# Performance work log

Hardware: AMD Instinct MI355X
Metric: run time of the kernel (lower is better)

The kernel has to match this reference:

```python
import jax, jax.numpy as jnp
import numpy as np

B, C, H, W = 8, 256, 64, 64
S = 2            # area_size = sqrt(num_areas)
A = S * S        # num_areas
NH = 8           # num_heads (hardcoded in module)
EPS = 1e-5       # nn.LayerNorm default eps


def setup_inputs() -> dict:
    key = jax.random.key(0)
    ks = jax.random.split(key, 4)
    scale = 0.02
    return {
        "x": jax.random.normal(ks[0], (B, C, H, W), jnp.float32),
        "W_in": jax.random.normal(ks[1], (A, 3 * C, C), jnp.float32) * scale,
        "b_in": jnp.zeros((A, 3 * C), jnp.float32),
        "W_out": jax.random.normal(ks[2], (A, C, C), jnp.float32) * scale,
        "b_out": jnp.zeros((A, C), jnp.float32),
        "gamma": jnp.ones((C,), jnp.float32),
        "beta": jnp.zeros((C,), jnp.float32),
    }


def reference(x, W_in, b_in, W_out, b_out, gamma, beta):
    b, c, h, w = x.shape
    ah, aw = h // S, w // S
    L = ah * aw
    dh = c // NH

    # split into 2x2 areas, flatten each to a sequence: [B, A, L, C]
    # area index = i*S + j (row-major), matching the torch loop order
    xa = (x.reshape(b, c, S, ah, S, aw)
            .transpose(0, 2, 4, 3, 5, 1)   # [B, i, j, ah, aw, C]
            .reshape(b, A, L, c))

    # per-area in-projection (torch Linear: y = x @ W^T + b)
    qkv = jnp.einsum('balc,adc->bald', xa, W_in) + b_in[None, :, None, :]
    q, k, v = jnp.split(qkv, 3, axis=-1)
    q = q.reshape(b, A, L, NH, dh)
    k = k.reshape(b, A, L, NH, dh)
    v = v.reshape(b, A, L, NH, dh)

    scale = jnp.asarray(dh, x.dtype) ** -0.5
    scores = jnp.einsum('balhd,bamhd->bahlm', q * scale, k)  # [B,A,NH,L,L]
    attn = jax.nn.softmax(scores, axis=-1)
    o = jnp.einsum('bahlm,bamhd->balhd', attn, v).reshape(b, A, L, c)
    o = jnp.einsum('balc,adc->bald', o, W_out) + b_out[None, :, None, :]

    # residual + shared LayerNorm over channel dim
    y = o + xa
    mu = jnp.mean(y, axis=-1, keepdims=True)
    var = jnp.mean((y - mu) ** 2, axis=-1, keepdims=True)
    y = (y - mu) * jax.lax.rsqrt(var + EPS) * gamma + beta

    # reassemble areas back to [B, C, H, W]
    out = (y.reshape(b, S, S, ah, aw, c)
             .transpose(0, 5, 1, 3, 2, 4)  # [B, C, i, ah, j, aw]
             .reshape(b, c, h, w))
    return out
```

## Files before the change

kernel.cpp:

```cpp
#include <hip/hip_runtime.h>
#include <cstdint>
#include <cstddef>

#define B_    8
#define C_    256
#define H_    64
#define W_    64
#define A_    4
#define NH_   8
#define DH_   32
#define L_    1024
#define NPAIR 32
#define QKVN  768

typedef __bf16 bf16;
typedef __bf16 bf16x8 __attribute__((ext_vector_type(8)));
typedef __bf16 bf16x4 __attribute__((ext_vector_type(4)));
typedef float  f32x4  __attribute__((ext_vector_type(4)));

#define QSCALE 0.25506866729736328f

__device__ inline f32x4 mfma16(bf16x8 a, bf16x8 b, f32x4 c) {
    return __builtin_amdgcn_mfma_f32_16x16x32_bf16(a, b, c, 0, 0, 0);
}
__device__ inline bf16x8 ld8(const bf16* p) { return *(const bf16x8*)p; }

__device__ inline void stage16(const bf16* g, bf16* l) {
    __builtin_amdgcn_global_load_lds(
        (const __attribute__((address_space(1))) void*)g,
        (__attribute__((address_space(3))) void*)l, 16, 0, 0);
}

#define NW4 (786432 / 4)
#define NO4 (262144 / 4)
__global__ __launch_bounds__(256) void k_split(const float* __restrict__ x,
                                               bf16* __restrict__ xa,
                                               const float* __restrict__ Win,
                                               const float* __restrict__ Wout,
                                               bf16* __restrict__ Winb,
                                               bf16* __restrict__ Woutb) {
    __shared__ float lds[32][257];
    int bid = blockIdx.x;
    int t = threadIdx.x;
    if (bid >= NPAIR * 32) {
        int tid = (bid - NPAIR * 32) * 256 + t;
        if (tid < NW4) {
            float4 v = ((const float4*)Win)[tid];
            bf16x4 ov = {(bf16)v.x, (bf16)v.y, (bf16)v.z, (bf16)v.w};
            ((bf16x4*)Winb)[tid] = ov;
        } else if (tid < NW4 + NO4) {
            int t2 = tid - NW4;
            float4 v = ((const float4*)Wout)[t2];
            bf16x4 ov = {(bf16)v.x, (bf16)v.y, (bf16)v.z, (bf16)v.w};
            ((bf16x4*)Woutb)[t2] = ov;
        }
        return;
    }
    int pair = bid >> 5, p = bid & 31;
    int b = pair >> 2, a = pair & 3, i = a >> 1, j = a & 1;
    int q = t & 31, csub = t >> 5;
    const float* xb = x + (size_t)b * C_ * H_ * W_ + (size_t)(i * 32 + p) * W_ + j * 32;
    for (int r = 0; r < 32; ++r) {
        int c = r * 8 + csub;
        lds[q][c] = xb[(size_t)c * H_ * W_ + q];
    }
    __syncthreads();
    bf16* xr = xa + ((size_t)pair * L_ + (size_t)p * 32) * C_;
    for (int r = 0; r < 32; ++r) {
        xr[(size_t)r * C_ + t] = (bf16)lds[r][t];
    }
}

__global__ __launch_bounds__(256) void k_qkv(const bf16* __restrict__ xa,
                                             const bf16* __restrict__ Win,
                                             const float* __restrict__ bin,
                                             bf16* __restrict__ qk,
                                             bf16* __restrict__ vT) {
    __shared__ __align__(16) char smem[32768];
    bf16* lA = (bf16*)smem;
    bf16* lB = (bf16*)(smem + 16384);
    int bid = blockIdx.x;
    int nt = bid % 6, mt = (bid / 6) & 7, pair = bid / 48;
    int a = pair & 3;
    int t = threadIdx.x, w = t >> 6, lane = t & 63;
    int wm = w >> 1, wn = w & 1;
    int quad = lane >> 4, l16 = lane & 15;
    int m0 = mt * 128, n0 = nt * 128;
    int r8 = lane >> 3, pc = lane & 7, jj = pc ^ r8;
    const bf16* ga = xa + (size_t)pair * L_ * C_ + (size_t)(m0 + w * 32 + r8) * C_ + jj * 8;
    const bf16* gb = Win + (size_t)a * QKVN * C_ + (size_t)(n0 + w * 32 + r8) * C_ + jj * 8;
    f32x4 acc[4][4];
#pragma unroll
    for (int fm = 0; fm < 4; ++fm)
#pragma unroll
        for (int fn = 0; fn < 4; ++fn) acc[fm][fn] = (f32x4){0.f, 0.f, 0.f, 0.f};
#pragma unroll
    for (int i = 0; i < 4; ++i) {
        stage16(ga + (size_t)(i * 8) * C_, lA + (w * 32 + i * 8) * 64);
        stage16(gb + (size_t)(i * 8) * C_, lB + (w * 32 + i * 8) * 64);
    }
    for (int k0 = 0; k0 < C_; k0 += 64) {
        __syncthreads();
        bf16x8 am[2][4], bn[2][4];
#pragma unroll
        for (int ks = 0; ks < 2; ++ks) {
            int p = (ks * 4 + quad) ^ (l16 & 7);
#pragma unroll
            for (int f = 0; f < 4; ++f) {
                am[ks][f] = *(const bf16x8*)&lA[(wm * 64 + f * 16 + l16) * 64 + p * 8];
                bn[ks][f] = *(const bf16x8*)&lB[(wn * 64 + f * 16 + l16) * 64 + p * 8];
            }
        }
        __syncthreads();
        if (k0 + 64 < C_) {
            int kn = k0 + 64;
#pragma unroll
            for (int i = 0; i < 4; ++i) {
                stage16(ga + (size_t)(i * 8) * C_ + kn, lA + (w * 32 + i * 8) * 64);
                stage16(gb + (size_t)(i * 8) * C_ + kn, lB + (w * 32 + i * 8) * 64);
            }
        }
#pragma unroll
        for (int ks = 0; ks < 2; ++ks)
#pragma unroll
            for (int fm = 0; fm < 4; ++fm)
#pragma unroll
                for (int fn = 0; fn < 4; ++fn)
                    acc[fm][fn] = mfma16(am[ks][fm], bn[ks][fn], acc[fm][fn]);
    }
    int colbase = n0 + wn * 64;
    int mb = m0 + wm * 64;
    __syncthreads();
    bf16* slab = (bf16*)smem + w * 2304;
    float bias[4];
#pragma unroll
    for (int fn = 0; fn < 4; ++fn) bias[fn] = bin[a * QKVN + colbase + fn * 16 + l16];
    int sr = lane >> 3, seg = lane & 7;
    if (colbase < 512) {
        float sc = (colbase < 256) ? QSCALE : 1.0f;
        bf16* ob = qk + (size_t)pair * L_ * 512;
#pragma unroll
        for (int pass = 0; pass < 2; ++pass) {
#pragma unroll
            for (int k = 0; k < 2; ++k) {
                int fm = pass * 2 + k;
#pragma unroll
                for (int fn = 0; fn < 4; ++fn)
#pragma unroll
                    for (int r = 0; r < 4; ++r)
                        slab[(k * 16 + quad * 4 + r) * 72 + fn * 16 + l16] =
                            (bf16)((acc[fm][fn][r] + bias[fn]) * sc);
            }
#pragma unroll
            for (int rr = 0; rr < 4; ++rr) {
                int row = rr * 8 + sr;
                bf16x8 v = *(const bf16x8*)&slab[row * 72 + seg * 8];
                *(bf16x8*)&ob[(size_t)(mb + pass * 32 + row) * 512 + colbase + seg * 8] = v;
            }
        }
    } else {
        bf16* vb = vT + (size_t)pair * C_ * L_;
        int e00 = colbase - 512;
#pragma unroll
        for (int pass = 0; pass < 2; ++pass) {
#pragma unroll
            for (int k = 0; k < 2; ++k) {
                int fn = pass * 2 + k;
#pragma unroll
                for (int fm = 0; fm < 4; ++fm) {
                    bf16x4 pk = {(bf16)(acc[fm][fn][0] + bias[fn]), (bf16)(acc[fm][fn][1] + bias[fn]),
                                 (bf16)(acc[fm][fn][2] + bias[fn]), (bf16)(acc[fm][fn][3] + bias[fn])};
                    *(bf16x4*)&slab[(k * 16 + l16) * 72 + fm * 16 + quad * 4] = pk;
                }
            }
#pragma unroll
            for (int rr = 0; rr < 4; ++rr) {
                int el = rr * 8 + sr;
                bf16x8 v = *(const bf16x8*)&slab[el * 72 + seg * 8];
                *(bf16x8*)&vb[(size_t)(e00 + pass * 32 + el) * L_ + mb + seg * 8] = v;
            }
        }
    }
}

__global__ __launch_bounds__(256) void k_attn(const bf16* __restrict__ qk,
                                              const bf16* __restrict__ vT,
                                              bf16* __restrict__ o) {
    __shared__ __align__(16) bf16 pl[4][1024];
    __shared__ __align__(16) bf16 klds[4 * 512];
    __shared__ __align__(16) bf16 vlds[4 * 512];
    int bid = blockIdx.x;
    int pair = bid & 31, rest = bid >> 5;
    int head = rest & 7, qb = rest >> 3;
    int t = threadIdx.x, w = t >> 6, lane = t & 63, quad = lane >> 4, l16 = lane & 15;
    const bf16* qbp = qk + (size_t)pair * L_ * 512;
    const bf16* kg = qbp + (size_t)(l16 * 4 + w) * 512 + 256 + head * DH_ + quad * 8;
    const bf16* vg = vT + ((size_t)pair * C_ + head * DH_ + (w & 1) * 16 + l16) * L_
                        + (w >> 1) * 32 + quad * 8;
    bf16* kdst = &klds[w * 512];
    bf16* vdst = &vlds[w * 512];
    int qbase = qb * 128 + w * 32;
    bf16x8 qf[2];
    f32x4 acc0[2], acc1[2], l4[2];
#pragma unroll
    for (int f = 0; f < 2; ++f) {
        qf[f] = ld8(qbp + (size_t)(qbase + f * 16 + l16) * 512 + head * DH_ + quad * 8);
        acc0[f] = (f32x4){0.f, 0.f, 0.f, 0.f};
        acc1[f] = (f32x4){0.f, 0.f, 0.f, 0.f};
        l4[f]   = (f32x4){0.f, 0.f, 0.f, 0.f};
    }
    stage16(kg, kdst);
    stage16(vg, vdst);
    __syncthreads();

    for (int kv0 = 0; kv0 < L_; kv0 += 64) {
        bf16x8 kf[4], vf[4];
#pragma unroll
        for (int i = 0; i < 4; ++i) {
            kf[i] = ld8(&klds[(i * 64 + lane) * 8]);
            vf[i] = ld8(&vlds[(i * 64 + lane) * 8]);
        }
        __syncthreads();
        int kvn = (kv0 + 64) & (L_ - 1);
        stage16(kg + (size_t)kvn * 512, kdst);
        stage16(vg + kvn, vdst);
#pragma unroll
        for (int f = 0; f < 2; ++f) {
            f32x4 s[4];
#pragma unroll
            for (int kb = 0; kb < 4; ++kb) s[kb] = mfma16(qf[f], kf[kb], (f32x4){0.f, 0.f, 0.f, 0.f});
            char* pw = (char*)&pl[w][0];
#pragma unroll
            for (int r = 0; r < 4; ++r) {
                float p0 = __builtin_amdgcn_exp2f(s[0][r]);
                float p1 = __builtin_amdgcn_exp2f(s[1][r]);
                float p2 = __builtin_amdgcn_exp2f(s[2][r]);
                float p3 = __builtin_amdgcn_exp2f(s[3][r]);
                l4[f][r] += (p0 + p1) + (p2 + p3);
                bf16x4 pv = {(bf16)p0, (bf16)p1, (bf16)p2, (bf16)p3};
                int row = quad * 4 + r;
                int wo = (row * 128 + l16 * 8) ^ ((row & 7) << 4);
                *(bf16x4*)(pw + wo) = pv;
            }
#pragma unroll
            for (int ks = 0; ks < 2; ++ks) {
                int ro = (l16 * 128 + ks * 64 + quad * 16) ^ ((l16 & 7) << 4);
                bf16x8 pf = *(const bf16x8*)(pw + ro);
                acc0[f] = mfma16(pf, vf[ks * 2 + 0], acc0[f]);
                acc1[f] = mfma16(pf, vf[ks * 2 + 1], acc1[f]);
            }
        }
        __syncthreads();
    }
    bf16* orow = o + (size_t)pair * L_ * C_ + head * DH_;
#pragma unroll
    for (int f = 0; f < 2; ++f) {
#pragma unroll
        for (int r = 0; r < 4; ++r) {
            float s1 = l4[f][r];
#pragma unroll
            for (int off = 1; off < 16; off <<= 1) s1 += __shfl_xor(s1, off);
            float inv = 1.f / s1;
            int row = qbase + f * 16 + quad * 4 + r;
            orow[(size_t)row * C_ + l16]      = (bf16)(acc0[f][r] * inv);
            orow[(size_t)row * C_ + 16 + l16] = (bf16)(acc1[f][r] * inv);
        }
    }
}

__global__ __launch_bounds__(256) void k_out(const bf16* __restrict__ o,
                                             const bf16* __restrict__ Wout,
                                             const float* __restrict__ bout,
                                             const bf16* __restrict__ xa,
                                             const float* __restrict__ gamma,
                                             const float* __restrict__ beta,
                                             float* __restrict__ out) {
    __shared__ __align__(16) char smem[40960];
    bf16* lA = (bf16*)smem;
    bf16* lB = (bf16*)(smem + 8192);
    float* tr = (float*)smem;
    __shared__ float red[2][2][32][2];
    int bid = blockIdx.x;
    int mt = bid & 15, pair = bid >> 4;
    int a = pair & 3;
    int t = threadIdx.x, w = t >> 6, lane = t & 63;
    int wm = w >> 1, wn = w & 1;
    int quad = lane >> 4, l16 = lane & 15;
    int m0 = mt * 64;
    int r8 = lane >> 3, pc = lane & 7, jj = pc ^ r8;
    const bf16* ga = o + (size_t)pair * L_ * C_ + (size_t)(m0 + w * 16 + r8) * C_ + jj * 8;
    const bf16* gb = Wout + (size_t)a * C_ * C_ + (size_t)(w * 64 + r8) * C_ + jj * 8;
    f32x4 acc[2][8];
#pragma unroll
    for (int fm = 0; fm < 2; ++fm)
#pragma unroll
        for (int fn = 0; fn < 8; ++fn) acc[fm][fn] = (f32x4){0.f, 0.f, 0.f, 0.f};
    for (int k0 = 0; k0 < C_; k0 += 64) {
        __syncthreads();
#pragma unroll
        for (int i = 0; i < 2; ++i)
            stage16(ga + (size_t)(i * 8) * C_ + k0, lA + (w * 16 + i * 8) * 64);
#pragma unroll
        for (int i = 0; i < 8; ++i)
            stage16(gb + (size_t)(i * 8) * C_ + k0, lB + (w * 64 + i * 8) * 64);
        __syncthreads();
#pragma unroll
        for (int ks = 0; ks < 2; ++ks) {
            int p = (ks * 4 + quad) ^ (l16 & 7);
            bf16x8 am[2], bn[8];
#pragma unroll
            for (int f = 0; f < 2; ++f)
                am[f] = *(const bf16x8*)&lA[(wm * 32 + f * 16 + l16) * 64 + p * 8];
#pragma unroll
            for (int f = 0; f < 8; ++f)
                bn[f] = *(const bf16x8*)&lB[(wn * 128 + f * 16 + l16) * 64 + p * 8];
#pragma unroll
            for (int fm = 0; fm < 2; ++fm)
#pragma unroll
                for (int fn = 0; fn < 8; ++fn)
                    acc[fm][fn] = mfma16(am[fm], bn[fn], acc[fm][fn]);
        }
    }
    const bf16* xb = xa + ((size_t)pair * L_ + m0 + wm * 32) * C_;
    float g8[8], be8[8];
#pragma unroll
    for (int fn = 0; fn < 8; ++fn) {
        int col = wn * 128 + fn * 16 + l16;
        float bias = bout[a * C_ + col];
        g8[fn] = gamma[col];
        be8[fn] = beta[col];
#pragma unroll
        for (int fm = 0; fm < 2; ++fm)
#pragma unroll
            for (int r = 0; r < 4; ++r)
                acc[fm][fn][r] += bias + (float)xb[(size_t)(fm * 16 + quad * 4 + r) * C_ + col];
    }
#pragma unroll
    for (int fm = 0; fm < 2; ++fm) {
#pragma unroll
        for (int r = 0; r < 4; ++r) {
            float s1 = 0.f, s2 = 0.f;
#pragma unroll
            for (int fn = 0; fn < 8; ++fn) {
                float v = acc[fm][fn][r];
                s1 += v; s2 += v * v;
            }
#pragma unroll
            for (int off = 1; off < 16; off <<= 1) {
                s1 += __shfl_xor(s1, off);
                s2 += __shfl_xor(s2, off);
            }
            if (l16 == 0) {
                int rl = fm * 16 + quad * 4 + r;
                red[wm][wn][rl][0] = s1;
                red[wm][wn][rl][1] = s2;
            }
        }
    }
    __syncthreads();
#pragma unroll
    for (int fm = 0; fm < 2; ++fm) {
#pragma unroll
        for (int r = 0; r < 4; ++r) {
            int rl = fm * 16 + quad * 4 + r;
            float t1 = red[wm][0][rl][0] + red[wm][1][rl][0];
            float t2 = red[wm][0][rl][1] + red[wm][1][rl][1];
            float mu = t1 * (1.f / 256.f);
            float var = t2 * (1.f / 256.f) - mu * mu;
            float rstd = rsqrtf(var + 1e-5f);
#pragma unroll
            for (int fn = 0; fn < 8; ++fn)
                acc[fm][fn][r] = (acc[fm][fn][r] - mu) * rstd * g8[fn] + be8[fn];
        }
    }
    int b = pair >> 2, i = (a >> 1), j = a & 1;
    int q = t & 31, csub = t >> 5;
    float* ob = out + (size_t)b * C_ * H_ * W_ + (size_t)(i * 32 + (m0 >> 5)) * W_ + j * 32;
#pragma unroll
    for (int ch = 0; ch < 2; ++ch) {
        __syncthreads();
        if (wm == ch) {
#pragma unroll
            for (int fm = 0; fm < 2; ++fm) {
                int rb = fm * 16 + quad * 4;
#pragma unroll
                for (int r = 0; r < 4; ++r)
#pragma unroll
                    for (int fn = 0; fn < 8; ++fn)
                        tr[(rb + r) * 258 + wn * 128 + fn * 16 + l16] = acc[fm][fn][r];
            }
        }
        __syncthreads();
#pragma unroll
        for (int r32 = 0; r32 < 32; ++r32) {
            int c = r32 * 8 + csub;
            ob[(size_t)c * (H_ * W_) + (size_t)ch * W_ + q] = tr[q * 258 + c];
        }
    }
}

extern "C" void kernel_launch(void* const* d_in, const int* in_sizes, int n_in,
                              void* d_out, int out_size, void* d_ws, size_t ws_size,
                              hipStream_t stream) {
    (void)in_sizes; (void)n_in; (void)out_size; (void)ws_size;
    const float* x     = (const float*)d_in[0];
    const float* Win   = (const float*)d_in[1];
    const float* bin   = (const float*)d_in[2];
    const float* Wout  = (const float*)d_in[3];
    const float* bout  = (const float*)d_in[4];
    const float* gamma = (const float*)d_in[5];
    const float* beta  = (const float*)d_in[6];
    float* out = (float*)d_out;

    char* ws = (char*)d_ws;
    bf16* xa    = (bf16*)ws;
    bf16* qk    = (bf16*)(ws + ((size_t)16 << 20));
    bf16* vT    = (bf16*)(ws + ((size_t)48 << 20));
    bf16* o     = (bf16*)(ws + ((size_t)64 << 20));
    bf16* Winb  = (bf16*)(ws + ((size_t)80 << 20));
    bf16* Woutb = (bf16*)(ws + ((size_t)82 << 20));

    k_split<<<NPAIR * 32 + 1024, 256, 0, stream>>>(x, xa, Win, Wout, Winb, Woutb);
    k_qkv<<<NPAIR * 8 * 6, 256, 0, stream>>>(xa, Winb, bin, qk, vT);
    k_attn<<<NPAIR * NH_ * 8, 256, 0, stream>>>(qk, vT, o);
    k_out<<<NPAIR * 16, 256, 0, stream>>>(o, Woutb, bout, xa, gamma, beta, out);
}
```

Before: 193.9 us.

## Halve out-projection tile and load GEMM operands directly from global memory

The output projection + LayerNorm kernel now handles 32 rows per block instead of 64, which doubles the grid to 1024 blocks. Its MFMA operands are loaded straight from global memory (ld8) instead of being staged through swizzled shared memory. This removes the per-k-step barriers and LDS staging, and the transpose store now runs in a single pass. In exchange, each block rereads the full Wout slice from global/L2 with less reuse, and the smaller tile halves the MFMA work per operand load.

```diff
diff --git a/kernel.cpp b/kernel.cpp
--- a/kernel.cpp
+++ b/kernel.cpp
@@ -275,53 +275,36 @@
                                              const float* __restrict__ gamma,
                                              const float* __restrict__ beta,
                                              float* __restrict__ out) {
-    __shared__ __align__(16) char smem[40960];
-    bf16* lA = (bf16*)smem;
-    bf16* lB = (bf16*)(smem + 8192);
-    float* tr = (float*)smem;
-    __shared__ float red[2][2][32][2];
+    __shared__ float tr[32 * 258];
+    __shared__ float red[2][2][16][2];
     int bid = blockIdx.x;
-    int mt = bid & 15, pair = bid >> 4;
+    int mt = bid & 31, pair = bid >> 5;
     int a = pair & 3;
     int t = threadIdx.x, w = t >> 6, lane = t & 63;
     int wm = w >> 1, wn = w & 1;
     int quad = lane >> 4, l16 = lane & 15;
-    int m0 = mt * 64;
-    int r8 = lane >> 3, pc = lane & 7, jj = pc ^ r8;
-    const bf16* ga = o + (size_t)pair * L_ * C_ + (size_t)(m0 + w * 16 + r8) * C_ + jj * 8;
-    const bf16* gb = Wout + (size_t)a * C_ * C_ + (size_t)(w * 64 + r8) * C_ + jj * 8;
-    f32x4 acc[2][8];
-#pragma unroll
-    for (int fm = 0; fm < 2; ++fm)
-#pragma unroll
-        for (int fn = 0; fn < 8; ++fn) acc[fm][fn] = (f32x4){0.f, 0.f, 0.f, 0.f};
+    int m0 = mt * 32;
+    const bf16* ga = o + (size_t)pair * L_ * C_ + (size_t)(m0 + wm * 16 + l16) * C_;
+    const bf16* gb = Wout + (size_t)a * C_ * C_ + (size_t)(wn * 128 + l16) * C_;
+    f32x4 acc[8];
+#pragma unroll
+    for (int fn = 0; fn < 8; ++fn) acc[fn] = (f32x4){0.f, 0.f, 0.f, 0.f};
+#pragma unroll 1
     for (int k0 = 0; k0 < C_; k0 += 64) {
-        __syncthreads();
-#pragma unroll
-        for (int i = 0; i < 2; ++i)
-            stage16(ga + (size_t)(i * 8) * C_ + k0, lA + (w * 16 + i * 8) * 64);
-#pragma unroll
-        for (int i = 0; i < 8; ++i)
-            stage16(gb + (size_t)(i * 8) * C_ + k0, lB + (w * 64 + i * 8) * 64);
-        __syncthreads();
 #pragma unroll
         for (int ks = 0; ks < 2; ++ks) {
-            int p = (ks * 4 + quad) ^ (l16 & 7);
-            bf16x8 am[2], bn[8];
-#pragma unroll
-            for (int f = 0; f < 2; ++f)
-                am[f] = *(const bf16x8*)&lA[(wm * 32 + f * 16 + l16) * 64 + p * 8];
+            int kk = k0 + ks * 32 + quad * 8;
+            bf16x8 am = ld8(ga + kk);
+            bf16x8 bn[8];
 #pragma unroll
             for (int f = 0; f < 8; ++f)
-                bn[f] = *(const bf16x8*)&lB[(wn * 128 + f * 16 + l16) * 64 + p * 8];
-#pragma unroll
-            for (int fm = 0; fm < 2; ++fm)
-#pragma unroll
-                for (int fn = 0; fn < 8; ++fn)
-                    acc[fm][fn] = mfma16(am[fm], bn[fn], acc[fm][fn]);
-        }
-    }
-    const bf16* xb = xa + ((size_t)pair * L_ + m0 + wm * 32) * C_;
+                bn[f] = ld8(gb + (size_t)(f * 16) * C_ + kk);
+#pragma unroll
+            for (int fn = 0; fn < 8; ++fn)
+                acc[fn] = mfma16(am, bn[fn], acc[fn]);
+        }
+    }
+    const bf16* xb = xa + ((size_t)pair * L_ + m0 + wm * 16) * C_;
     float g8[8], be8[8];
 #pragma unroll
     for (int fn = 0; fn < 8; ++fn) {
@@ -330,72 +313,50 @@
         g8[fn] = gamma[col];
         be8[fn] = beta[col];
 #pragma unroll
-        for (int fm = 0; fm < 2; ++fm)
-#pragma unroll
-            for (int r = 0; r < 4; ++r)
-                acc[fm][fn][r] += bias + (float)xb[(size_t)(fm * 16 + quad * 4 + r) * C_ + col];
-    }
-#pragma unroll
-    for (int fm = 0; fm < 2; ++fm) {
-#pragma unroll
-        for (int r = 0; r < 4; ++r) {
-            float s1 = 0.f, s2 = 0.f;
-#pragma unroll
-            for (int fn = 0; fn < 8; ++fn) {
-                float v = acc[fm][fn][r];
-                s1 += v; s2 += v * v;
-            }
-#pragma unroll
-            for (int off = 1; off < 16; off <<= 1) {
-                s1 += __shfl_xor(s1, off);
-                s2 += __shfl_xor(s2, off);
-            }
-            if (l16 == 0) {
-                int rl = fm * 16 + quad * 4 + r;
-                red[wm][wn][rl][0] = s1;
-                red[wm][wn][rl][1] = s2;
-            }
-        }
-    }
-    __syncthreads();
-#pragma unroll
-    for (int fm = 0; fm < 2; ++fm) {
-#pragma unroll
-        for (int r = 0; r < 4; ++r) {
-            int rl = fm * 16 + quad * 4 + r;
-            float t1 = red[wm][0][rl][0] + red[wm][1][rl][0];
-            float t2 = red[wm][0][rl][1] + red[wm][1][rl][1];
-            float mu = t1 * (1.f / 256.f);
-            float var = t2 * (1.f / 256.f) - mu * mu;
-            float rstd = rsqrtf(var + 1e-5f);
-#pragma unroll
-            for (int fn = 0; fn < 8; ++fn)
-                acc[fm][fn][r] = (acc[fm][fn][r] - mu) * rstd * g8[fn] + be8[fn];
-        }
-    }
+        for (int r = 0; r < 4; ++r)
+            acc[fn][r] += bias + (float)xb[(size_t)(quad * 4 + r) * C_ + col];
+    }
+#pragma unroll
+    for (int r = 0; r < 4; ++r) {
+        float s1 = 0.f, s2 = 0.f;
+#pragma unroll
+        for (int fn = 0; fn < 8; ++fn) {
+            float v = acc[fn][r];
+            s1 += v; s2 += v * v;
+        }
+#pragma unroll
+        for (int off = 1; off < 16; off <<= 1) {
+            s1 += __shfl_xor(s1, off);
+            s2 += __shfl_xor(s2, off);
+        }
+        if (l16 == 0) {
+            red[wm][wn][quad * 4 + r][0] = s1;
+            red[wm][wn][quad * 4 + r][1] = s2;
+        }
+    }
+    __syncthreads();
+#pragma unroll
+    for (int r = 0; r < 4; ++r) {
+        int rl = quad * 4 + r;
+        float t1 = red[wm][0][rl][0] + red[wm][1][rl][0];
+        float t2 = red[wm][0][rl][1] + red[wm][1][rl][1];
+        float mu = t1 * (1.f / 256.f);
+        float var = t2 * (1.f / 256.f) - mu * mu;
+        float rstd = rsqrtf(var + 1e-5f);
+#pragma unroll
+        for (int fn = 0; fn < 8; ++fn) {
+            float v = (acc[fn][r] - mu) * rstd * g8[fn] + be8[fn];
+            tr[(wm * 16 + rl) * 258 + wn * 128 + fn * 16 + l16] = v;
+        }
+    }
+    __syncthreads();
     int b = pair >> 2, i = (a >> 1), j = a & 1;
     int q = t & 31, csub = t >> 5;
-    float* ob = out + (size_t)b * C_ * H_ * W_ + (size_t)(i * 32 + (m0 >> 5)) * W_ + j * 32;
-#pragma unroll
-    for (int ch = 0; ch < 2; ++ch) {
-        __syncthreads();
-        if (wm == ch) {
-#pragma unroll
-            for (int fm = 0; fm < 2; ++fm) {
-                int rb = fm * 16 + quad * 4;
-#pragma unroll
-                for (int r = 0; r < 4; ++r)
-#pragma unroll
-                    for (int fn = 0; fn < 8; ++fn)
-                        tr[(rb + r) * 258 + wn * 128 + fn * 16 + l16] = acc[fm][fn][r];
-            }
-        }
-        __syncthreads();
-#pragma unroll
-        for (int r32 = 0; r32 < 32; ++r32) {
-            int c = r32 * 8 + csub;
-            ob[(size_t)c * (H_ * W_) + (size_t)ch * W_ + q] = tr[q * 258 + c];
-        }
+    float* ob = out + (size_t)b * C_ * H_ * W_ + (size_t)(i * 32 + mt) * W_ + j * 32;
+#pragma unroll
+    for (int r32 = 0; r32 < 32; ++r32) {
+        int c = r32 * 8 + csub;
+        ob[(size_t)c * (H_ * W_) + q] = tr[q * 258 + c];
     }
 }
 
@@ -423,5 +384,5 @@
     k_split<<<NPAIR * 32 + 1024, 256, 0, stream>>>(x, xa, Win, Wout, Winb, Woutb);
     k_qkv<<<NPAIR * 8 * 6, 256, 0, stream>>>(xa, Winb, bin, qk, vT);
     k_attn<<<NPAIR * NH_ * 8, 256, 0, stream>>>(qk, vT, o);
-    k_out<<<NPAIR * 16, 256, 0, stream>>>(o, Woutb, bout, xa, gamma, beta, out);
-}
+    k_out<<<NPAIR * 32, 256, 0, stream>>>(o, Woutb, bout, xa, gamma, beta, out);
+}
```

Measured after the change: 214.9 us. +10.9%, slower.

## Rewrite attention kernel with 32x32 MFMA and register-resident P via permlane swaps

Applied to the files above, without the earlier changes.

The attention kernel switches from 16x16x32 MFMA tiles with LDS-staged K/V and an LDS round trip for the probability matrix to 32x32x16 MFMA computing S^T. The probabilities are packed to bf16 in registers and rearranged with v_permlane32_swap, so they feed the PV MFMA directly. K and V are now loaded straight from global memory each 32-key step instead of being staged through LDS, and all __syncthreads calls are removed. This is meant to cut LDS traffic and barrier stalls. In exchange, global loads are no longer shared across waves, so the kernel relies on cache hits and has less latency hiding.

```diff
diff --git a/kernel.cpp b/kernel.cpp
--- a/kernel.cpp
+++ b/kernel.cpp
@@ -17,13 +17,27 @@
 typedef __bf16 bf16x8 __attribute__((ext_vector_type(8)));
 typedef __bf16 bf16x4 __attribute__((ext_vector_type(4)));
 typedef float  f32x4  __attribute__((ext_vector_type(4)));
+typedef float  f32x16 __attribute__((ext_vector_type(16)));
+typedef int    i32x4  __attribute__((ext_vector_type(4)));
 
 #define QSCALE 0.25506866729736328f
 
 __device__ inline f32x4 mfma16(bf16x8 a, bf16x8 b, f32x4 c) {
     return __builtin_amdgcn_mfma_f32_16x16x32_bf16(a, b, c, 0, 0, 0);
 }
+__device__ inline f32x16 mfma32(bf16x8 a, bf16x8 b, f32x16 c) {
+    return __builtin_amdgcn_mfma_f32_32x32x16_bf16(a, b, c, 0, 0, 0);
+}
 __device__ inline bf16x8 ld8(const bf16* p) { return *(const bf16x8*)p; }
+
+__device__ inline int cvtpk(float lo, float hi) {
+    int r;
+    asm("v_cvt_pk_bf16_f32 %0, %1, %2" : "=v"(r) : "v"(lo), "v"(hi));
+    return r;
+}
+__device__ inline void swap32(int& a, int& b) {
+    asm volatile("v_permlane32_swap_b32 %0, %1" : "+v"(a), "+v"(b));
+}
 
 __device__ inline void stage16(const bf16* g, bf16* l) {
     __builtin_amdgcn_global_load_lds(
@@ -186,85 +200,62 @@
 __global__ __launch_bounds__(256) void k_attn(const bf16* __restrict__ qk,
                                               const bf16* __restrict__ vT,
                                               bf16* __restrict__ o) {
-    __shared__ __align__(16) bf16 pl[4][1024];
-    __shared__ __align__(16) bf16 klds[4 * 512];
-    __shared__ __align__(16) bf16 vlds[4 * 512];
     int bid = blockIdx.x;
     int pair = bid & 31, rest = bid >> 5;
     int head = rest & 7, qb = rest >> 3;
-    int t = threadIdx.x, w = t >> 6, lane = t & 63, quad = lane >> 4, l16 = lane & 15;
+    int t = threadIdx.x, w = t >> 6, lane = t & 63;
+    int l31 = lane & 31, hi = lane >> 5;
+    int qrow = qb * 128 + w * 32 + l31;
     const bf16* qbp = qk + (size_t)pair * L_ * 512;
-    const bf16* kg = qbp + (size_t)(l16 * 4 + w) * 512 + 256 + head * DH_ + quad * 8;
-    const bf16* vg = vT + ((size_t)pair * C_ + head * DH_ + (w & 1) * 16 + l16) * L_
-                        + (w >> 1) * 32 + quad * 8;
-    bf16* kdst = &klds[w * 512];
-    bf16* vdst = &vlds[w * 512];
-    int qbase = qb * 128 + w * 32;
-    bf16x8 qf[2];
-    f32x4 acc0[2], acc1[2], l4[2];
-#pragma unroll
-    for (int f = 0; f < 2; ++f) {
-        qf[f] = ld8(qbp + (size_t)(qbase + f * 16 + l16) * 512 + head * DH_ + quad * 8);
-        acc0[f] = (f32x4){0.f, 0.f, 0.f, 0.f};
-        acc1[f] = (f32x4){0.f, 0.f, 0.f, 0.f};
-        l4[f]   = (f32x4){0.f, 0.f, 0.f, 0.f};
-    }
-    stage16(kg, kdst);
-    stage16(vg, vdst);
-    __syncthreads();
-
-    for (int kv0 = 0; kv0 < L_; kv0 += 64) {
-        bf16x8 kf[4], vf[4];
-#pragma unroll
-        for (int i = 0; i < 4; ++i) {
-            kf[i] = ld8(&klds[(i * 64 + lane) * 8]);
-            vf[i] = ld8(&vlds[(i * 64 + lane) * 8]);
-        }
-        __syncthreads();
-        int kvn = (kv0 + 64) & (L_ - 1);
-        stage16(kg + (size_t)kvn * 512, kdst);
-        stage16(vg + kvn, vdst);
-#pragma unroll
-        for (int f = 0; f < 2; ++f) {
-            f32x4 s[4];
-#pragma unroll
-            for (int kb = 0; kb < 4; ++kb) s[kb] = mfma16(qf[f], kf[kb], (f32x4){0.f, 0.f, 0.f, 0.f});
-            char* pw = (char*)&pl[w][0];
-#pragma unroll
-            for (int r = 0; r < 4; ++r) {
-                float p0 = __builtin_amdgcn_exp2f(s[0][r]);
-                float p1 = __builtin_amdgcn_exp2f(s[1][r]);
-                float p2 = __builtin_amdgcn_exp2f(s[2][r]);
-                float p3 = __builtin_amdgcn_exp2f(s[3][r]);
-                l4[f][r] += (p0 + p1) + (p2 + p3);
-                bf16x4 pv = {(bf16)p0, (bf16)p1, (bf16)p2, (bf16)p3};
-                int row = quad * 4 + r;
-                int wo = (row * 128 + l16 * 8) ^ ((row & 7) << 4);
-                *(bf16x4*)(pw + wo) = pv;
-            }
-#pragma unroll
-            for (int ks = 0; ks < 2; ++ks) {
-                int ro = (l16 * 128 + ks * 64 + quad * 16) ^ ((l16 & 7) << 4);
-                bf16x8 pf = *(const bf16x8*)(pw + ro);
-                acc0[f] = mfma16(pf, vf[ks * 2 + 0], acc0[f]);
-                acc1[f] = mfma16(pf, vf[ks * 2 + 1], acc1[f]);
-            }
-        }
-        __syncthreads();
-    }
-    bf16* orow = o + (size_t)pair * L_ * C_ + head * DH_;
-#pragma unroll
-    for (int f = 0; f < 2; ++f) {
-#pragma unroll
-        for (int r = 0; r < 4; ++r) {
-            float s1 = l4[f][r];
-#pragma unroll
-            for (int off = 1; off < 16; off <<= 1) s1 += __shfl_xor(s1, off);
-            float inv = 1.f / s1;
-            int row = qbase + f * 16 + quad * 4 + r;
-            orow[(size_t)row * C_ + l16]      = (bf16)(acc0[f][r] * inv);
-            orow[(size_t)row * C_ + 16 + l16] = (bf16)(acc1[f][r] * inv);
-        }
+    const bf16* qp = qbp + (size_t)qrow * 512 + head * DH_ + hi * 8;
+    const bf16* kb = qbp + (size_t)l31 * 512 + 256 + head * DH_ + hi * 8;
+    const bf16* vb = vT + ((size_t)pair * C_ + head * DH_ + l31) * L_ + hi * 8;
+    bf16x8 qf0 = ld8(qp);
+    bf16x8 qf1 = ld8(qp + 16);
+    f32x16 acc = {0.f, 0.f, 0.f, 0.f, 0.f, 0.f, 0.f, 0.f,
+                  0.f, 0.f, 0.f, 0.f, 0.f, 0.f, 0.f, 0.f};
+    float lsum = 0.f;
+    for (int kv0 = 0; kv0 < L_; kv0 += 32) {
+        bf16x8 ka0 = ld8(kb + (size_t)kv0 * 512);
+        bf16x8 ka1 = ld8(kb + (size_t)kv0 * 512 + 16);
+        bf16x8 va0 = ld8(vb + kv0);
+        bf16x8 va1 = ld8(vb + kv0 + 16);
+        f32x16 s = {0.f, 0.f, 0.f, 0.f, 0.f, 0.f, 0.f, 0.f,
+                    0.f, 0.f, 0.f, 0.f, 0.f, 0.f, 0.f, 0.f};
+        s = mfma32(ka0, qf0, s);
+        s = mfma32(ka1, qf1, s);
+        float e0  = __builtin_amdgcn_exp2f(s[0]),  e1  = __builtin_amdgcn_exp2f(s[1]);
+        float e2  = __builtin_amdgcn_exp2f(s[2]),  e3  = __builtin_amdgcn_exp2f(s[3]);
+        float e4  = __builtin_amdgcn_exp2f(s[4]),  e5  = __builtin_amdgcn_exp2f(s[5]);
+        float e6  = __builtin_amdgcn_exp2f(s[6]),  e7  = __builtin_amdgcn_exp2f(s[7]);
+        float e8  = __builtin_amdgcn_exp2f(s[8]),  e9  = __builtin_amdgcn_exp2f(s[9]);
+        float e10 = __builtin_amdgcn_exp2f(s[10]), e11 = __builtin_amdgcn_exp2f(s[11]);
+        float e12 = __builtin_amdgcn_exp2f(s[12]), e13 = __builtin_amdgcn_exp2f(s[13]);
+        float e14 = __builtin_amdgcn_exp2f(s[14]), e15 = __builtin_amdgcn_exp2f(s[15]);
+        lsum += (((e0 + e1) + (e2 + e3)) + ((e4 + e5) + (e6 + e7))) +
+                (((e8 + e9) + (e10 + e11)) + ((e12 + e13) + (e14 + e15)));
+        int a1 = cvtpk(e0, e1), a2 = cvtpk(e2, e3);
+        int b1 = cvtpk(e4, e5), b2 = cvtpk(e6, e7);
+        swap32(a1, b1);
+        swap32(a2, b2);
+        i32x4 f0 = {a1, a2, b1, b2};
+        acc = mfma32(va0, __builtin_bit_cast(bf16x8, f0), acc);
+        int c1 = cvtpk(e8, e9),   c2 = cvtpk(e10, e11);
+        int d1 = cvtpk(e12, e13), d2 = cvtpk(e14, e15);
+        swap32(c1, d1);
+        swap32(c2, d2);
+        i32x4 f1 = {c1, c2, d1, d2};
+        acc = mfma32(va1, __builtin_bit_cast(bf16x8, f1), acc);
+    }
+    float la = lsum, lb = lsum;
+    asm volatile("v_permlane32_swap_b32 %0, %1" : "+v"(la), "+v"(lb));
+    float inv = 1.f / (la + lb);
+    bf16* orow = o + ((size_t)pair * L_ + qrow) * C_ + head * DH_;
+#pragma unroll
+    for (int g = 0; g < 4; ++g) {
+        bf16x4 ov = {(bf16)(acc[4 * g + 0] * inv), (bf16)(acc[4 * g + 1] * inv),
+                     (bf16)(acc[4 * g + 2] * inv), (bf16)(acc[4 * g + 3] * inv)};
+        *(bf16x4*)&orow[8 * g + 4 * hi] = ov;
     }
 }
 
```

After: 271.8 us. +40.2%, slower.
